# Kernel optimization log

Measured on AMD Instinct MI355X. Metric: run time of the kernel, lower is better.

Reference implementation:

```python
import jax, jax.numpy as jnp
import numpy as np
from jax import lax

CLS_POW = 1.0
IOU_POW = 6.0
TOP_K = 15
CLS_CNT = 80
B, M, K = 32, 64, 8400
EPS = 1e-7


def _ciou(box1, box2):
    # box1, box2: broadcastable xyxy boxes -> CIoU, shape = broadcast(...)[:-1]
    b1x1, b1y1, b1x2, b1y2 = (box1[..., i] for i in range(4))
    b2x1, b2y1, b2x2, b2y2 = (box2[..., i] for i in range(4))
    w1, h1 = b1x2 - b1x1, b1y2 - b1y1
    w2, h2 = b2x2 - b2x1, b2y2 - b2y1
    iw = jnp.clip(jnp.minimum(b1x2, b2x2) - jnp.maximum(b1x1, b2x1), 0.0)
    ih = jnp.clip(jnp.minimum(b1y2, b2y2) - jnp.maximum(b1y1, b2y1), 0.0)
    inter = iw * ih
    union = w1 * h1 + w2 * h2 - inter + EPS
    iou = inter / union
    cw = jnp.maximum(b1x2, b2x2) - jnp.minimum(b1x1, b2x1)  # enclosing box
    ch = jnp.maximum(b1y2, b2y2) - jnp.minimum(b1y1, b2y1)
    c2 = cw * cw + ch * ch + EPS
    rho2 = ((b2x1 + b2x2 - b1x1 - b1x2) ** 2 + (b2y1 + b2y2 - b1y1 - b1y2) ** 2) / 4.0
    v = (4.0 / (np.pi ** 2)) * (jnp.arctan(w2 / (h2 + EPS)) - jnp.arctan(w1 / (h1 + EPS))) ** 2
    alpha = v / (v - iou + (1.0 + EPS))
    return iou - (rho2 / c2 + alpha * v)


def setup_inputs() -> dict:
    key = jax.random.key(0)
    ks = jax.random.split(key, 8)
    points = jax.random.uniform(ks[0], (K, 2)) * 640.0
    cxy = jax.random.uniform(ks[1], (B, M, 2)) * 640.0
    wh = jax.random.uniform(ks[2], (B, M, 2)) * 180.0 + 20.0
    gt_bboxes = jnp.clip(jnp.concatenate([cxy - wh / 2, cxy + wh / 2], -1), 0.0, 640.0)
    gt_labels = jax.random.randint(ks[3], (B, M, 1), 0, CLS_CNT)
    pcxy = points[None] + jax.random.normal(ks[4], (B, K, 2)) * 8.0
    pwh = jax.random.uniform(ks[5], (B, K, 2)) * 180.0 + 20.0
    pred_bboxes = jnp.concatenate([pcxy - pwh / 2, pcxy + pwh / 2], -1)
    pred_scores = jax.random.uniform(ks[6], (B, K, CLS_CNT))
    n_valid = jax.random.randint(ks[7], (B,), 1, M + 1)
    gt_mask = jnp.arange(M)[None, :] < n_valid[:, None]
    return {"points": points, "gt_bboxes": gt_bboxes, "gt_labels": gt_labels,
            "pred_bboxes": pred_bboxes, "pred_scores": pred_scores, "gt_mask": gt_mask}


def reference(points, gt_bboxes, gt_labels, pred_bboxes, pred_scores, gt_mask):
    b, m, _ = gt_bboxes.shape
    k = points.shape[0]
    labels = gt_labels[..., 0].astype(jnp.int32)  # (b, m)

    # 1. anchor-in-gt-box mask (b, m, k)
    mn, mx = gt_bboxes[:, :, None, :2], gt_bboxes[:, :, None, 2:]
    p = points[None, None]
    diff = jnp.concatenate([mn - p, p - mx], axis=-1)
    pos_mask = (diff.max(-1) < 1e-6) & gt_mask[:, :, None]
    posf = pos_mask.astype(pred_scores.dtype)

    # 2. alignment metrics: class score gathered at gt label * CIoU^pow
    idx = jnp.broadcast_to(labels[:, :, None, None], (b, m, k, 1))
    ts = jnp.take_along_axis(pred_scores[:, None], idx, axis=3)[..., 0] * posf  # (b,m,k)
    overlaps = jnp.clip(_ciou(gt_bboxes[:, :, None, :], pred_bboxes[:, None, :, :]), 0.0) * posf
    am = ts ** CLS_POW * overlaps ** IOU_POW

    # 3. top-k per gt box, dropping anchors selected more than once by scatter-count
    tkv, tki = lax.top_k(am, TOP_K)
    tkm = tkv > 1e-9
    tki = jnp.where(tkm, tki, 0)
    counts = jnp.zeros((b, m, k), jnp.int32).at[
        jnp.arange(b)[:, None, None], jnp.arange(m)[None, :, None], tki
    ].add(tkm.astype(jnp.int32))
    assign = (counts == 1).astype(jnp.int32)  # (b, m, k)

    # 4. resolve anchors assigned to multiple gts via max-overlap (matches torch `if`)
    fg0 = assign.sum(1)
    def _filter(a):
        mi = jnp.argmax(overlaps, axis=1)  # (b, k)
        mm = (jnp.arange(m)[None, :, None] == mi[:, None, :]).astype(a.dtype)
        return a * mm
    assign = lax.cond(jnp.max(fg0) > 1, _filter, lambda a: a, assign)
    fg = assign.sum(1)  # (b, k)

    # 5. target matrices
    tbi = jnp.argmax(assign, axis=1)  # (b, k)
    tgt_labels = jnp.take_along_axis(labels, tbi, axis=1)
    tgt_bboxes = jnp.take_along_axis(gt_bboxes, tbi[..., None], axis=1)
    onehot = jax.nn.one_hot(tgt_labels, CLS_CNT, dtype=gt_bboxes.dtype) * fg[..., None].astype(gt_bboxes.dtype)

    # 6. per-instance normalization of scores
    am_a = am * assign.astype(am.dtype)
    am_n = am_a / (am_a.max(-1, keepdims=True) + 1e-9) * overlaps.max(-1, keepdims=True)
    factor = am_n.max(axis=1)  # (b, k)
    tso = onehot * factor[..., None]
    return tso, tgt_bboxes, assign.astype(jnp.int8), overlaps, fg.astype(jnp.int8)
```

## Files before the change

### kernel.cpp

```cpp
#include <hip/hip_runtime.h>
#include <math.h>

constexpr int NB = 32, NM = 64, NK = 8400, NC = 80, NT = 15;
constexpr int NQ = 4, KQ = 2100;
constexpr float FEPS = 1e-7f;

typedef float f32x4 __attribute__((ext_vector_type(4)));

constexpr size_t OUT_TSO = 0;
constexpr size_t OUT_TGT = (size_t)NB * NK * NC;
constexpr size_t OUT_ASN = OUT_TGT + (size_t)NB * NK * 4;
constexpr size_t OUT_OVL = OUT_ASN + (size_t)NB * NM * NK;
constexpr size_t OUT_FG  = OUT_OVL + (size_t)NB * NM * NK;

constexpr int NCOMP = NB * NM * NQ;
constexpr int NFILL = 2048;
constexpr int N4A  = (int)(OUT_TGT / 4);
constexpr int N4B  = (int)((OUT_OVL - OUT_ASN) / 4);
constexpr int ASN4 = (int)(OUT_ASN / 4);
constexpr int TOT4 = N4A + N4B;
constexpr int S4   = 832;
constexpr int F4   = TOT4 - NCOMP * S4;

static __device__ __forceinline__ void fill_slice(float* out, int cidx, int t)
{
  f32x4* o4 = (f32x4*)out;
  const f32x4 z = {0.f, 0.f, 0.f, 0.f};
  const int base = F4 + cidx * S4;
  for (int j = base + (t - 64); j < base + S4; j += 192) {
    const int a = (j < N4A) ? j : (j - N4A + ASN4);
    __builtin_nontemporal_store(z, &o4[a]);
  }
}

__global__ __launch_bounds__(256) void kZ(unsigned long long* __restrict__ mikey,
                                          int* __restrict__ fg0,
                                          int* __restrict__ flag)
{
  const int n = NB * NK;
  const int tid = blockIdx.x * 256 + threadIdx.x;
  for (int i = tid; i < n; i += gridDim.x * 256) { mikey[i] = 0ULL; fg0[i] = 0; }
  if (tid == 0) *flag = 0;
}

__global__ __launch_bounds__(256) void kAF(
    const float* __restrict__ points, const float* __restrict__ gt_bboxes,
    const int* __restrict__ gt_labels, const float* __restrict__ pred_bboxes,
    const float* __restrict__ pred_scores, const int* __restrict__ gt_mask,
    float* __restrict__ out, unsigned long long* __restrict__ candk,
    float* __restrict__ ovmaxq, unsigned long long* __restrict__ mikey)
{
  __shared__ __align__(16) float s_ov[KQ];
  __shared__ unsigned short s_pos[KQ];
  __shared__ float s_cv[KQ];
  __shared__ unsigned short s_ci[KQ];
  __shared__ int   s_np, s_cnt;
  __shared__ float s_m[4];

  const int bx = blockIdx.x;
  const int t  = threadIdx.x;

  if ((bx % 5) == 4) {
    const int fidx = bx / 5;
    f32x4* o4 = (f32x4*)out;
    const f32x4 z = {0.f, 0.f, 0.f, 0.f};
    for (int j = fidx * 256 + t; j < F4; j += NFILL * 256) {
      const int a = (j < N4A) ? j : (j - N4A + ASN4);
      __builtin_nontemporal_store(z, &o4[a]);
    }
    return;
  }

  const int cidx = bx - (bx + 1) / 5;
  const int bm = cidx >> 2;
  const int q  = cidx & 3;
  const int b  = bm >> 6;
  const int m  = bm & 63;
  const int wid = t >> 6, lane = t & 63;
  const int kbeg = q * KQ;

  unsigned long long* ck = candk + (size_t)(bm * NQ + q) * NT;
  float* ovl_out = out + OUT_OVL + (size_t)bm * NK;
  f32x4* ov4 = (f32x4*)(ovl_out + kbeg);

  const int maskv = gt_mask[bm];
  if (!maskv) {
    const f32x4 z = {0.f, 0.f, 0.f, 0.f};
    for (int idx = t; idx < KQ / 4; idx += 256)
      __builtin_nontemporal_store(z, &ov4[idx]);
    if (wid != 0) { fill_slice(out, cidx, t); return; }
    if (t == 0) ovmaxq[bm * NQ + q] = 0.f;
    if (lane < NT) ck[lane] = 0ULL;
    return;
  }
  if (t == 0) { s_np = 0; s_cnt = 0; }
  __syncthreads();

  const float4 g = *(const float4*)(gt_bboxes + (size_t)bm * 4);
  const int   label = gt_labels[bm];
  const float2* pts = (const float2*)points;

  #pragma unroll
  for (int j = 0; j < 9; ++j) {
    const int idx = j * 256 + t;
    if (idx < KQ) {
      s_ov[idx] = 0.f;
      const int k = kbeg + idx;
      float2 p = pts[k];
      float dmax = fmaxf(fmaxf(g.x - p.x, g.y - p.y),
                         fmaxf(p.x - g.z, p.y - g.w));
      if (dmax < 1e-6f) {
        int e = atomicAdd(&s_np, 1);
        s_pos[e] = (unsigned short)idx;
      }
    }
  }
  __syncthreads();
  const int np = s_np;

  const float4* pb = (const float4*)(pred_bboxes + (size_t)b * NK * 4);
  const float*  ps = pred_scores + (size_t)b * NK * NC;
  unsigned long long* mk = mikey + (size_t)b * NK;

  const float w1 = g.z - g.x, h1 = g.w - g.y;
  const float at1 = atanf(w1 / (h1 + FEPS));
  const float area1 = w1 * h1;
  const float CV = (float)(4.0 / (M_PI * M_PI));
  const float ONE_EPS = (float)(1.0 + 1e-7);

  float lmax = 0.f;
  for (int e = t; e < np; e += 256) {
    const int li = s_pos[e];
    const int k = kbeg + li;
    float4 qb = pb[k];
    float w2 = qb.z - qb.x, h2 = qb.w - qb.y;
    float iw = fmaxf(fminf(g.z, qb.z) - fmaxf(g.x, qb.x), 0.f);
    float ih = fmaxf(fminf(g.w, qb.w) - fmaxf(g.y, qb.y), 0.f);
    float inter = iw * ih;
    float uni = area1 + w2 * h2 - inter + FEPS;
    float iou = inter / uni;
    float cw = fmaxf(g.z, qb.z) - fminf(g.x, qb.x);
    float ch = fmaxf(g.w, qb.w) - fminf(g.y, qb.y);
    float c2 = cw * cw + ch * ch + FEPS;
    float ex = qb.x + qb.z - g.x - g.z;
    float ey = qb.y + qb.w - g.y - g.w;
    float rho2 = (ex * ex + ey * ey) * 0.25f;
    float dat = atanf(w2 / (h2 + FEPS)) - at1;
    float v = CV * dat * dat;
    float alpha = v / (v - iou + ONE_EPS);
    float ciou = iou - (rho2 / c2 + alpha * v);
    float ov = fmaxf(ciou, 0.f);
    if (ov > 0.f) {
      s_ov[li] = ov;
      unsigned long long key =
          ((unsigned long long)__float_as_uint(ov) << 32) |
          (unsigned long long)(NM - 1 - m);
      atomicMax(&mk[k], key);
      lmax = fmaxf(lmax, ov);
      float ts = ps[(size_t)k * NC + label];
      float o2 = ov * ov;
      float am = ts * (o2 * o2 * o2);
      if (am > 1e-9f) {
        int p2 = atomicAdd(&s_cnt, 1);
        s_cv[p2] = am;
        s_ci[p2] = (unsigned short)li;
      }
    }
  }

  float mv = lmax;
  #pragma unroll
  for (int d = 1; d < 64; d <<= 1) mv = fmaxf(mv, __shfl_xor(mv, d));
  if (lane == 0) s_m[wid] = mv;
  __syncthreads();
  if (t == 0)
    ovmaxq[bm * NQ + q] = fmaxf(fmaxf(s_m[0], s_m[1]), fmaxf(s_m[2], s_m[3]));

  const f32x4* sv4 = (const f32x4*)s_ov;
  for (int idx = t; idx < KQ / 4; idx += 256)
    __builtin_nontemporal_store(sv4[idx], &ov4[idx]);

  if (wid != 0) { fill_slice(out, cidx, t); return; }

  const int n = s_cnt;

  if (n <= NT) {
    if (lane < NT) {
      unsigned long long key = 0ULL;
      if (lane < n) {
        const int gk = kbeg + s_ci[lane];
        key = ((unsigned long long)__float_as_uint(s_cv[lane]) << 32) |
              (unsigned long long)(0xFFFFFFFFu - (unsigned)gk);
      }
      ck[lane] = key;
    }
    return;
  }

  unsigned long long bkey = 0; int bslot = -1;
  for (int e = lane; e < n; e += 64) {
    float v = s_cv[e];
    unsigned long long key =
        ((unsigned long long)__float_as_uint(v) << 32) |
        (unsigned long long)(0xFFFFu - s_ci[e]);
    if (key > bkey) { bkey = key; bslot = e; }
  }
  for (int it = 0; it < NT; ++it) {
    unsigned long long wkey = bkey;
    #pragma unroll
    for (int d = 1; d < 64; d <<= 1) {
      unsigned long long ok = __shfl_xor(wkey, d);
      if (ok > wkey) wkey = ok;
    }
    if (lane == 0) {
      const int gk = kbeg + (int)(0xFFFFu - (unsigned)(wkey & 0xFFFFu));
      ck[it] = (wkey & 0xFFFFFFFF00000000ull) |
               (unsigned long long)(0xFFFFFFFFu - (unsigned)gk);
    }
    if (bkey == wkey) {
      s_cv[bslot] = -1.f;
      bkey = 0; bslot = -1;
      for (int e = lane; e < n; e += 64) {
        float v = s_cv[e];
        if (v >= 0.f) {
          unsigned long long key =
              ((unsigned long long)__float_as_uint(v) << 32) |
              (unsigned long long)(0xFFFFu - s_ci[e]);
          if (key > bkey) { bkey = key; bslot = e; }
        }
      }
    }
  }
}

__global__ __launch_bounds__(64) void kA2(
    const unsigned long long* __restrict__ candk,
    const float* __restrict__ ovmaxq, float* __restrict__ ovmaxp,
    int* __restrict__ tki, float* __restrict__ tkv,
    int* __restrict__ fg0, int* __restrict__ flag)
{
  const int bm = blockIdx.x;
  const int b  = bm >> 6;
  const int lane = threadIdx.x;

  if (lane == 0) {
    const float* om = ovmaxq + bm * NQ;
    ovmaxp[bm] = fmaxf(fmaxf(om[0], om[1]), fmaxf(om[2], om[3]));
  }

  unsigned long long mkey = (lane < NQ * NT)
      ? candk[(size_t)bm * NQ * NT + lane] : 0ULL;
  unsigned long long mywin = 0ULL;
  int nf = 0;
  for (int it = 0; it < NT; ++it) {
    unsigned long long wkey = mkey;
    #pragma unroll
    for (int d = 1; d < 64; d <<= 1) {
      unsigned long long ok = __shfl_xor(wkey, d);
      if (ok > wkey) wkey = ok;
    }
    if (wkey == 0) break;
    if (lane == it) mywin = wkey;
    if (mkey == wkey) mkey = 0ULL;
    nf = it + 1;
  }

  if (lane < NT) {
    if (lane < nf) {
      const int fi = (int)(0xFFFFFFFFu - (unsigned)mywin);
      tki[bm * NT + lane] = fi;
      tkv[bm * NT + lane] = __uint_as_float((unsigned)(mywin >> 32));
      int old = atomicAdd(&fg0[(size_t)b * NK + fi], 1);
      if (old >= 1) atomicOr(flag, 1);
    } else {
      tki[bm * NT + lane] = -1;
      tkv[bm * NT + lane] = 0.f;
    }
  }
}

__global__ __launch_bounds__(256) void kF(
    const float* __restrict__ gt_bboxes, const int* __restrict__ gt_labels,
    const int* __restrict__ tki, const float* __restrict__ tkv,
    const float* __restrict__ ovmaxp, const unsigned long long* __restrict__ mikey,
    const int* __restrict__ flagp, float* __restrict__ out)
{
  __shared__ int    s_tki[NM * NT];
  __shared__ float  s_tkv[NM * NT];
  __shared__ unsigned char s_keep[NM * NT];
  __shared__ float  s_rowmax[NM];
  __shared__ float  s_ovmax[NM];
  __shared__ int    s_label[NM];
  __shared__ f32x4  s_gtb[NM];
  __shared__ int    s_mk[256];
  __shared__ float  s_sv[256];

  const int b  = blockIdx.y;
  const int k0 = blockIdx.x * 256;
  const int t  = threadIdx.x;
  const int flag = *flagp;

  for (int e = t; e < NM * NT; e += 256) {
    s_tki[e] = tki[b * NM * NT + e];
    s_tkv[e] = tkv[b * NM * NT + e];
  }
  if (t < NM) {
    s_ovmax[t] = ovmaxp[b * NM + t];
    s_label[t] = gt_labels[b * NM + t];
    s_gtb[t] = *(const f32x4*)(gt_bboxes + (size_t)(b * NM + t) * 4);
  }
  s_mk[t] = -1;
  s_sv[t] = 0.f;
  __syncthreads();

  for (int e = t; e < NM * NT; e += 256) {
    const int idx = s_tki[e];
    bool kp = (idx >= 0);
    if (kp && flag) {
      unsigned long long key = mikey[(size_t)b * NK + idx];
      int mi = NM - 1 - (int)(key & 0xFFFFFFFFull);
      kp = (mi == e / NT);
    }
    s_keep[e] = kp;
  }
  __syncthreads();

  if (t < NM) {
    float r = 0.f;
    for (int j = 0; j < NT; ++j) {
      const int e = t * NT + j;
      if (s_keep[e]) r = fmaxf(r, s_tkv[e]);
    }
    s_rowmax[t] = r;
  }
  __syncthreads();

  for (int e = t; e < NM * NT; e += 256) {
    if (!s_keep[e]) continue;
    const int idx = s_tki[e];
    if (idx < k0 || idx >= k0 + 256) continue;
    const int m = e / NT;
    s_mk[idx - k0] = m;
    s_sv[idx - k0] = s_tkv[e] / (s_rowmax[m] + 1e-9f) * s_ovmax[m];
    out[OUT_ASN + (size_t)(b * NM + m) * NK + idx] = 1.f;
  }
  __syncthreads();

  const int k = k0 + t;
  if (k < NK) {
    const int mk2 = s_mk[t];
    const int tb = (mk2 >= 0) ? mk2 : 0;
    __builtin_nontemporal_store((mk2 >= 0) ? 1.f : 0.f,
                                &out[OUT_FG + (size_t)b * NK + k]);
    __builtin_nontemporal_store(s_gtb[tb],
        (f32x4*)(out + OUT_TGT + (size_t)(b * NK + k) * 4));
    if (mk2 >= 0)
      out[OUT_TSO + (size_t)(b * NK + k) * NC + s_label[mk2]] = s_sv[t];
  }
}

extern "C" void kernel_launch(void* const* d_in, const int* in_sizes, int n_in,
                              void* d_out, int out_size, void* d_ws, size_t ws_size,
                              hipStream_t stream)
{
  const float* points      = (const float*)d_in[0];
  const float* gt_bboxes   = (const float*)d_in[1];
  const int*   gt_labels   = (const int*)d_in[2];
  const float* pred_bboxes = (const float*)d_in[3];
  const float* pred_scores = (const float*)d_in[4];
  const int*   gt_mask     = (const int*)d_in[5];
  float* out = (float*)d_out;

  char* ws = (char*)d_ws;
  unsigned long long* mikey = (unsigned long long*)ws; ws += (size_t)NB * NK * 8;
  int*   fg0    = (int*)ws;    ws += (size_t)NB * NK * 4;
  int*   flag   = (int*)ws;    ws += 256;
  unsigned long long* candk = (unsigned long long*)ws;
                               ws += (size_t)NB * NM * NQ * NT * 8;
  int*   tki    = (int*)ws;    ws += (size_t)NB * NM * NT * 4;
  float* tkv    = (float*)ws;  ws += (size_t)NB * NM * NT * 4;
  float* ovmaxp = (float*)ws;  ws += (size_t)NB * NM * 4;
  float* ovmaxq = (float*)ws;  ws += (size_t)NB * NM * NQ * 4;

  kZ<<<1024, 256, 0, stream>>>(mikey, fg0, flag);

  kAF<<<NCOMP + NFILL, 256, 0, stream>>>(points, gt_bboxes, gt_labels,
                                         pred_bboxes, pred_scores, gt_mask,
                                         out, candk, ovmaxq, mikey);

  kA2<<<NB * NM, 64, 0, stream>>>(candk, ovmaxq, ovmaxp, tki, tkv, fg0, flag);

  dim3 g2((NK + 255) / 256, NB);
  kF<<<g2, 256, 0, stream>>>(gt_bboxes, gt_labels, tki, tkv, ovmaxp, mikey,
                             flag, out);
}
```

Before: 83.29 us.

## Scatter final targets per gt and fold dense tgt/fg fill into zero-fill

The dense per-anchor finalize kernel is replaced by a sparse per-gt kernel. Each (batch, gt) wave scatters only its kept top-k entries into the assign, fg, tgt_bboxes and score outputs. The default tgt_bboxes values (gt box 0 of the batch) and the zero fg values are now written by the existing fill blocks inside the compute kernel, so the final dense pass over all anchors goes away. The cost is a slightly larger fill slice with a per-element range check and a gt_bboxes load, plus scattered writes in the last kernel.

```diff
diff --git a/kernel.cpp b/kernel.cpp
--- a/kernel.cpp
+++ b/kernel.cpp
@@ -16,20 +16,26 @@
 constexpr int NCOMP = NB * NM * NQ;
 constexpr int NFILL = 2048;
 constexpr int N4A  = (int)(OUT_TGT / 4);
-constexpr int N4B  = (int)((OUT_OVL - OUT_ASN) / 4);
 constexpr int ASN4 = (int)(OUT_ASN / 4);
-constexpr int TOT4 = N4A + N4B;
-constexpr int S4   = 832;
+constexpr int OVL4 = (int)(OUT_OVL / 4);
+constexpr int FG4s = (int)(OUT_FG / 4);
+constexpr int FG4c = NB * NK / 4;
+constexpr int TOT4 = OVL4 + FG4c;
+constexpr int S4   = 960;
 constexpr int F4   = TOT4 - NCOMP * S4;
 
-static __device__ __forceinline__ void fill_slice(float* out, int cidx, int t)
+static __device__ __forceinline__ void zfill(float* out,
+                                             const float* __restrict__ gtb,
+                                             int j0, int j1, int step)
 {
   f32x4* o4 = (f32x4*)out;
   const f32x4 z = {0.f, 0.f, 0.f, 0.f};
-  const int base = F4 + cidx * S4;
-  for (int j = base + (t - 64); j < base + S4; j += 192) {
-    const int a = (j < N4A) ? j : (j - N4A + ASN4);
-    __builtin_nontemporal_store(z, &o4[a]);
+  for (int j = j0; j < j1; j += step) {
+    const int a = (j < OVL4) ? j : FG4s + (j - OVL4);
+    f32x4 v = z;
+    if (a >= N4A && a < ASN4)
+      v = *(const f32x4*)(gtb + (size_t)((a - N4A) / NK) * NM * 4);
+    __builtin_nontemporal_store(v, &o4[a]);
   }
 }
 
@@ -61,13 +67,7 @@
   const int t  = threadIdx.x;
 
   if ((bx % 5) == 4) {
-    const int fidx = bx / 5;
-    f32x4* o4 = (f32x4*)out;
-    const f32x4 z = {0.f, 0.f, 0.f, 0.f};
-    for (int j = fidx * 256 + t; j < F4; j += NFILL * 256) {
-      const int a = (j < N4A) ? j : (j - N4A + ASN4);
-      __builtin_nontemporal_store(z, &o4[a]);
-    }
+    zfill(out, gt_bboxes, (bx / 5) * 256 + t, F4, NFILL * 256);
     return;
   }
 
@@ -78,6 +78,7 @@
   const int m  = bm & 63;
   const int wid = t >> 6, lane = t & 63;
   const int kbeg = q * KQ;
+  const int sbase = F4 + cidx * S4;
 
   unsigned long long* ck = candk + (size_t)(bm * NQ + q) * NT;
   float* ovl_out = out + OUT_OVL + (size_t)bm * NK;
@@ -88,7 +89,7 @@
     const f32x4 z = {0.f, 0.f, 0.f, 0.f};
     for (int idx = t; idx < KQ / 4; idx += 256)
       __builtin_nontemporal_store(z, &ov4[idx]);
-    if (wid != 0) { fill_slice(out, cidx, t); return; }
+    if (wid != 0) { zfill(out, gt_bboxes, sbase + (t - 64), sbase + S4, 192); return; }
     if (t == 0) ovmaxq[bm * NQ + q] = 0.f;
     if (lane < NT) ck[lane] = 0ULL;
     return;
@@ -180,7 +181,7 @@
   for (int idx = t; idx < KQ / 4; idx += 256)
     __builtin_nontemporal_store(sv4[idx], &ov4[idx]);
 
-  if (wid != 0) { fill_slice(out, cidx, t); return; }
+  if (wid != 0) { zfill(out, gt_bboxes, sbase + (t - 64), sbase + S4, 192); return; }
 
   const int n = s_cnt;
 
@@ -279,83 +280,41 @@
   }
 }
 
-__global__ __launch_bounds__(256) void kF(
+__global__ __launch_bounds__(64) void kFS(
     const float* __restrict__ gt_bboxes, const int* __restrict__ gt_labels,
     const int* __restrict__ tki, const float* __restrict__ tkv,
     const float* __restrict__ ovmaxp, const unsigned long long* __restrict__ mikey,
     const int* __restrict__ flagp, float* __restrict__ out)
 {
-  __shared__ int    s_tki[NM * NT];
-  __shared__ float  s_tkv[NM * NT];
-  __shared__ unsigned char s_keep[NM * NT];
-  __shared__ float  s_rowmax[NM];
-  __shared__ float  s_ovmax[NM];
-  __shared__ int    s_label[NM];
-  __shared__ f32x4  s_gtb[NM];
-  __shared__ int    s_mk[256];
-  __shared__ float  s_sv[256];
-
-  const int b  = blockIdx.y;
-  const int k0 = blockIdx.x * 256;
-  const int t  = threadIdx.x;
+  const int bm = blockIdx.x;
+  const int b  = bm >> 6;
+  const int m  = bm & 63;
+  const int lane = threadIdx.x;
   const int flag = *flagp;
 
-  for (int e = t; e < NM * NT; e += 256) {
-    s_tki[e] = tki[b * NM * NT + e];
-    s_tkv[e] = tkv[b * NM * NT + e];
-  }
-  if (t < NM) {
-    s_ovmax[t] = ovmaxp[b * NM + t];
-    s_label[t] = gt_labels[b * NM + t];
-    s_gtb[t] = *(const f32x4*)(gt_bboxes + (size_t)(b * NM + t) * 4);
-  }
-  s_mk[t] = -1;
-  s_sv[t] = 0.f;
-  __syncthreads();
-
-  for (int e = t; e < NM * NT; e += 256) {
-    const int idx = s_tki[e];
-    bool kp = (idx >= 0);
-    if (kp && flag) {
-      unsigned long long key = mikey[(size_t)b * NK + idx];
-      int mi = NM - 1 - (int)(key & 0xFFFFFFFFull);
-      kp = (mi == e / NT);
-    }
-    s_keep[e] = kp;
-  }
-  __syncthreads();
-
-  if (t < NM) {
-    float r = 0.f;
-    for (int j = 0; j < NT; ++j) {
-      const int e = t * NT + j;
-      if (s_keep[e]) r = fmaxf(r, s_tkv[e]);
-    }
-    s_rowmax[t] = r;
-  }
-  __syncthreads();
-
-  for (int e = t; e < NM * NT; e += 256) {
-    if (!s_keep[e]) continue;
-    const int idx = s_tki[e];
-    if (idx < k0 || idx >= k0 + 256) continue;
-    const int m = e / NT;
-    s_mk[idx - k0] = m;
-    s_sv[idx - k0] = s_tkv[e] / (s_rowmax[m] + 1e-9f) * s_ovmax[m];
+  int idx = -1; float v = 0.f; bool keep = false;
+  if (lane < NT) {
+    idx = tki[bm * NT + lane];
+    if (idx >= 0) {
+      v = tkv[bm * NT + lane];
+      keep = true;
+      if (flag) {
+        unsigned long long key = mikey[(size_t)b * NK + idx];
+        keep = (NM - 1 - (int)(key & 0xFFFFFFFFull)) == m;
+      }
+    }
+  }
+  float r = keep ? v : 0.f;
+  #pragma unroll
+  for (int d = 1; d < 16; d <<= 1) r = fmaxf(r, __shfl_xor(r, d));
+
+  if (keep) {
+    const float sval = v / (r + 1e-9f) * ovmaxp[bm];
     out[OUT_ASN + (size_t)(b * NM + m) * NK + idx] = 1.f;
-  }
-  __syncthreads();
-
-  const int k = k0 + t;
-  if (k < NK) {
-    const int mk2 = s_mk[t];
-    const int tb = (mk2 >= 0) ? mk2 : 0;
-    __builtin_nontemporal_store((mk2 >= 0) ? 1.f : 0.f,
-                                &out[OUT_FG + (size_t)b * NK + k]);
-    __builtin_nontemporal_store(s_gtb[tb],
-        (f32x4*)(out + OUT_TGT + (size_t)(b * NK + k) * 4));
-    if (mk2 >= 0)
-      out[OUT_TSO + (size_t)(b * NK + k) * NC + s_label[mk2]] = s_sv[t];
+    out[OUT_TSO + (size_t)(b * NK + idx) * NC + gt_labels[bm]] = sval;
+    out[OUT_FG + (size_t)b * NK + idx] = 1.f;
+    *(f32x4*)(out + OUT_TGT + (size_t)(b * NK + idx) * 4) =
+        *(const f32x4*)(gt_bboxes + (size_t)bm * 4);
   }
 }
 
@@ -390,7 +349,6 @@
 
   kA2<<<NB * NM, 64, 0, stream>>>(candk, ovmaxq, ovmaxp, tki, tkv, fg0, flag);
 
-  dim3 g2((NK + 255) / 256, NB);
-  kF<<<g2, 256, 0, stream>>>(gt_bboxes, gt_labels, tki, tkv, ovmaxp, mikey,
-                             flag, out);
-}
+  kFS<<<NB * NM, 64, 0, stream>>>(gt_bboxes, gt_labels, tki, tkv, ovmaxp,
+                                  mikey, flag, out);
+}
```

New measurement: 77.88 us, median of 2. 6.5% less time.
